# Optimization experiments

Hardware: AMD Instinct MI355X
Metric: run time of the kernel (lower is better)

## Reference

```python
import jax, jax.numpy as jnp
import numpy as np

D_IN, D, H, NE, NPATCH, B = 768, 512, 4, 2048, 49, 512
DH = D // H


def _match(q, k, w, b):
    # q:[N,Lq,D], k:[N,Lk,D] -> cross-attention of q over k, then linear proj
    s = jnp.einsum('nqd,nkd->nqk', q, k) * (q.shape[-1] ** -0.5)
    a = jax.nn.softmax(s, axis=-1)
    return jnp.einsum('nqk,nkd->nqd', a, k) @ w + b


def _mh_pool(x, query, wq, bq, wk, bk, wv, bv, wo, bo):
    # multi-head attention pooling with 1 learned query -> [N, D]
    N, P, _ = x.shape
    q = (query @ wq + bq).reshape(H, 1, DH)                      # [H,1,dh]
    k = (x @ wk + bk).reshape(N, P, H, DH).transpose(0, 2, 1, 3)  # [N,H,P,dh]
    v = (x @ wv + bv).reshape(N, P, H, DH).transpose(0, 2, 1, 3)
    s = jnp.einsum('hqd,nhkd->nhqk', q, k) * (DH ** -0.5)
    a = jax.nn.softmax(s, axis=-1)
    o = jnp.einsum('nhqk,nhkd->nhqd', a, v).transpose(0, 2, 1, 3).reshape(N, D)
    return o @ wo + bo


def _ln(x, g, b):
    m = jnp.mean(x, -1, keepdims=True)
    v = jnp.var(x, -1, keepdims=True)
    return (x - m) * jax.lax.rsqrt(v + 1e-5) * g + b


def _moe(t, i, gw, gb, tw1, tb1, tw2, tb2, iw1, ib1, iw2, ib2):
    # 2-expert softmax-gated combiner over (text, pooled image) features
    gate = jax.nn.softmax(jnp.concatenate([t, i], -1) @ gw + gb, axis=-1)  # [N,2]
    et = jax.nn.relu(t @ tw1 + tb1) @ tw2 + tb2
    ei = jax.nn.relu(i @ iw1 + ib1) @ iw2 + ib2
    return gate[:, :1] * et + gate[:, 1:] * ei


def setup_inputs():
    key = jax.random.key(0)
    ks = jax.random.split(key, 24)
    g = lambda i, sh, s=0.02: jax.random.normal(ks[i], sh, dtype=jnp.float32) * s
    z = lambda *sh: jnp.zeros(sh, jnp.float32)
    return dict(
        entity_text_cls=g(0, (NE, D_IN), 1.0),
        entity_image_tokens=g(1, (NE, NPATCH, D_IN), 1.0),
        mention_text_cls=g(2, (B, D_IN), 1.0),
        mention_image_tokens=g(3, (B, NPATCH, D_IN), 1.0),
        text_fc_w=g(4, (D_IN, D)), text_fc_b=z(D),
        image_fc_w=g(5, (D_IN, D)), image_fc_b=z(D),
        gate_fc_w=g(6, (D, 1)), gate_fc_b=z(1),
        ln_g=jnp.ones((D,), jnp.float32), ln_b=z(D),
        match_w=g(7, (D, D)), match_b=z(D),
        mh_query=g(8, (1, D)),
        mh_wq=g(9, (D, D)), mh_bq=z(D),
        mh_wk=g(10, (D, D)), mh_bk=z(D),
        mh_wv=g(11, (D, D)), mh_bv=z(D),
        mh_wo=g(12, (D, D)), mh_bo=z(D),
        moe_gw=g(13, (2 * D, 2)), moe_gb=z(2),
        moe_tw1=g(14, (D, D)), moe_tb1=z(D),
        moe_tw2=g(15, (D, D)), moe_tb2=z(D),
        moe_iw1=g(16, (D, D)), moe_ib1=z(D),
        moe_iw2=g(17, (D, D)), moe_ib2=z(D),
    )


def reference(entity_text_cls, entity_image_tokens, mention_text_cls, mention_image_tokens,
              text_fc_w, text_fc_b, image_fc_w, image_fc_b, gate_fc_w, gate_fc_b,
              ln_g, ln_b, match_w, match_b, mh_query,
              mh_wq, mh_bq, mh_wk, mh_bk, mh_wv, mh_bv, mh_wo, mh_bo,
              moe_gw, moe_gb, moe_tw1, moe_tb1, moe_tw2, moe_tb2,
              moe_iw1, moe_ib1, moe_iw2, moe_ib2):
    def side(cls, toks):
        cls_p = cls @ text_fc_w + text_fc_b          # [N,D]
        tok_p = toks @ image_fc_w + image_fc_b       # [N,P,D]
        txt = _match(cls_p[:, None, :], tok_p, match_w, match_b)[:, 0]
        img = _match(tok_p, cls_p[:, None, :], match_w, match_b)
        img = _mh_pool(img, mh_query, mh_wq, mh_bq, mh_wk, mh_bk, mh_wv, mh_bv, mh_wo, mh_bo)
        ctx = _moe(txt, img, moe_gw, moe_gb, moe_tw1, moe_tb1, moe_tw2, moe_tb2,
                   moe_iw1, moe_ib1, moe_iw2, moe_ib2)
        gate = jnp.tanh(cls_p @ gate_fc_w + gate_fc_b)
        return _ln(cls_p * gate + ctx, ln_g, ln_b)

    e_ctx = side(entity_text_cls, entity_image_tokens)   # [NE,D]
    m_ctx = side(mention_text_cls, mention_image_tokens)  # [B,D]
    return m_ctx @ e_ctx.T                                # [B,NE]
```

## Files before the change

kernel.cpp:

```cpp
#include <hip/hip_runtime.h>
#include <hip/hip_bf16.h>
#include <math.h>

namespace {
constexpr int kNE   = 2048;
constexpr int kB    = 512;
constexpr int kDin  = 768;
constexpr int kD    = 512;
constexpr int kP    = 49;
constexpr int kNtot = kNE + kB;
}

typedef __attribute__((ext_vector_type(8))) short bf16x8;
typedef __attribute__((ext_vector_type(4))) float f32x4;

__device__ inline ushort f2bf(float f) {
  unsigned u = __float_as_uint(f);
  return (ushort)((u + 0x7fffu + ((u >> 16) & 1u)) >> 16);
}
__device__ inline void split1(float v, ushort& h, ushort& l) {
  unsigned u = __float_as_uint(v);
  h = (ushort)(u >> 16);
  l = f2bf(v - __uint_as_float(u & 0xFFFF0000u));
}

struct GemmJob {
  const ushort *Ah, *Al;
  const ushort *Bh, *Bl;
  const float* bias;
  float* Cf;
  ushort *Ch, *Cl;
  int M, N, K, relu;
};
struct GemmBatch { GemmJob j[4]; int prefix[5]; };

__global__ __launch_bounds__(256) void gemm_batch(GemmBatch batch) {
  int ji = 0;
  { const int bid = blockIdx.x;
    while (ji < 3 && bid >= batch.prefix[ji + 1]) ++ji; }
  const GemmJob jb = batch.j[ji];
  const int local = blockIdx.x - batch.prefix[ji];
  const int nbx = jb.N >> 7;
  const int by = local / nbx;
  const int bx = local - by * nbx;
  const int row0 = by * 64, col0 = bx * 128;
  const int K = jb.K;
  const int nt = K >> 5;

  __shared__ ushort Ahs[2][64][40], Als[2][64][40];
  __shared__ ushort Bhs[2][128][40], Bls[2][128][40];

  const int tid  = threadIdx.x;
  const int lane = tid & 63;
  const int w    = tid >> 6;
  const int fr   = lane & 15;
  const int fk   = (lane >> 4) * 8;
  const int sr   = tid >> 2;
  const int sk   = (tid & 3) * 8;

  const ushort* pAh  = jb.Ah + (size_t)(row0 + sr) * K + sk;
  const ushort* pAl  = jb.Al + (size_t)(row0 + sr) * K + sk;
  const ushort* pBh0 = jb.Bh + (size_t)(col0 + sr) * K + sk;
  const ushort* pBl0 = jb.Bl + (size_t)(col0 + sr) * K + sk;
  const ushort* pBh1 = jb.Bh + (size_t)(col0 + 64 + sr) * K + sk;
  const ushort* pBl1 = jb.Bl + (size_t)(col0 + 64 + sr) * K + sk;

  bf16x8 rAh, rAl, rBh0, rBl0, rBh1, rBl1;
  auto LOAD = [&](int t) {
    const int o = t * 32;
    rAh  = *(const bf16x8*)(pAh + o);  rAl  = *(const bf16x8*)(pAl + o);
    rBh0 = *(const bf16x8*)(pBh0 + o); rBl0 = *(const bf16x8*)(pBl0 + o);
    rBh1 = *(const bf16x8*)(pBh1 + o); rBl1 = *(const bf16x8*)(pBl1 + o);
  };
  auto STORE = [&](int b) {
    *(bf16x8*)&Ahs[b][sr][sk] = rAh;       *(bf16x8*)&Als[b][sr][sk] = rAl;
    *(bf16x8*)&Bhs[b][sr][sk] = rBh0;      *(bf16x8*)&Bls[b][sr][sk] = rBl0;
    *(bf16x8*)&Bhs[b][64 + sr][sk] = rBh1; *(bf16x8*)&Bls[b][64 + sr][sk] = rBl1;
  };

  f32x4 acc[4][2] = {};

  LOAD(0); STORE(0);
  if (nt > 1) LOAD(1);
  __syncthreads();

  for (int t = 0; t < nt; ++t) {
    const int cur = t & 1;
    bf16x8 bh[2], bl[2];
#pragma unroll
    for (int n = 0; n < 2; ++n) {
      bh[n] = *(const bf16x8*)&Bhs[cur][w * 32 + n * 16 + fr][fk];
      bl[n] = *(const bf16x8*)&Bls[cur][w * 32 + n * 16 + fr][fk];
    }
#pragma unroll
    for (int m = 0; m < 4; ++m) {
      bf16x8 ah = *(const bf16x8*)&Ahs[cur][m * 16 + fr][fk];
      bf16x8 al = *(const bf16x8*)&Als[cur][m * 16 + fr][fk];
#pragma unroll
      for (int n = 0; n < 2; ++n) {
        acc[m][n] = __builtin_amdgcn_mfma_f32_16x16x32_bf16(ah, bh[n], acc[m][n], 0, 0, 0);
        acc[m][n] = __builtin_amdgcn_mfma_f32_16x16x32_bf16(al, bh[n], acc[m][n], 0, 0, 0);
        acc[m][n] = __builtin_amdgcn_mfma_f32_16x16x32_bf16(ah, bl[n], acc[m][n], 0, 0, 0);
      }
    }
    if (t + 1 < nt) {
      STORE(cur ^ 1);
      if (t + 2 < nt) LOAD(t + 2);
    }
    __syncthreads();
  }

  const int fq = lane >> 4;
#pragma unroll
  for (int n = 0; n < 2; ++n) {
    const int col = col0 + w * 32 + n * 16 + fr;
    const float bv = jb.bias ? jb.bias[col] : 0.f;
#pragma unroll
    for (int m = 0; m < 4; ++m) {
      const int rbase = row0 + m * 16 + fq * 4;
#pragma unroll
      for (int jj = 0; jj < 4; ++jj) {
        float v = acc[m][n][jj] + bv;
        if (jb.relu) v = fmaxf(v, 0.f);
        const size_t idx = (size_t)(rbase + jj) * jb.N + col;
        if (jb.Cf) jb.Cf[idx] = v;
        if (jb.Ch) { ushort h, l; split1(v, h, l); jb.Ch[idx] = h; jb.Cl[idx] = l; }
      }
    }
  }
}

struct SplitJob { const float* src; ushort* hi; ushort* lo; int n4; };
struct SplitArgs { SplitJob j[5]; };
__global__ __launch_bounds__(256) void split_plain(SplitArgs a) {
  const SplitJob jb = a.j[blockIdx.y];
  const int i = blockIdx.x * 256 + threadIdx.x;
  if (i >= jb.n4) return;
  float4 v = *(const float4*)&jb.src[(size_t)i * 4];
  ushort4 h, l;
  split1(v.x, h.x, l.x); split1(v.y, h.y, l.y);
  split1(v.z, h.z, l.z); split1(v.w, h.w, l.w);
  *(ushort4*)&jb.hi[(size_t)i * 4] = h;
  *(ushort4*)&jb.lo[(size_t)i * 4] = l;
}

struct TSJob { const float* src; ushort* hi; ushort* lo; int R, C; };
struct TSArgs { TSJob j[7]; };
__global__ __launch_bounds__(256) void trans_split(TSArgs a) {
  const TSJob jb = a.j[blockIdx.z];
  const int r0 = blockIdx.y * 32, c0 = blockIdx.x * 32;
  if (r0 >= jb.R || c0 >= jb.C) return;
  __shared__ float tl[32][33];
  const int tx = threadIdx.x & 31, ty = threadIdx.x >> 5;
#pragma unroll
  for (int i = 0; i < 32; i += 8)
    tl[ty + i][tx] = jb.src[(size_t)(r0 + ty + i) * jb.C + c0 + tx];
  __syncthreads();
#pragma unroll
  for (int i = 0; i < 32; i += 8) {
    ushort h, l; split1(tl[tx][ty + i], h, l);
    const size_t idx = (size_t)(c0 + ty + i) * jb.R + r0 + tx;
    jb.hi[idx] = h; jb.lo[idx] = l;
  }
}

__global__ __launch_bounds__(256) void attn_pool(
    const float* __restrict__ ent_toks, const float* __restrict__ men_toks,
    const float* __restrict__ u, ushort* __restrict__ wh, ushort* __restrict__ wl) {
  const int n = blockIdx.x;
  const float* toks = (n < kNE) ? ent_toks + (size_t)n * kP * kDin
                                : men_toks + (size_t)(n - kNE) * kP * kDin;
  const float* un = u + (size_t)n * kDin;
  const int t = threadIdx.x;
  const int lane = t & 63, wave = t >> 6;

  const float u0 = un[t], u1 = un[t + 256], u2 = un[t + 512];

  __shared__ float rs[2][4];
  float m = -INFINITY, l = 0.f, a0 = 0.f, a1 = 0.f, a2 = 0.f;
  const float scale = 0.044194173824159216f;

  for (int p = 0; p < kP; ++p) {
    const float* tp = toks + (size_t)p * kDin;
    const float t0 = tp[t], t1 = tp[t + 256], t2 = tp[t + 512];
    float d = fmaf(t0, u0, fmaf(t1, u1, t2 * u2));
    for (int o = 32; o; o >>= 1) d += __shfl_xor(d, o);
    if (lane == 0) rs[p & 1][wave] = d;
    __syncthreads();
    const float s = (rs[p & 1][0] + rs[p & 1][1] + rs[p & 1][2] + rs[p & 1][3]) * scale;
    const float mn = fmaxf(m, s);
    const float c = __expf(m - mn);
    const float e = __expf(s - mn);
    l = l * c + e;
    a0 = fmaf(a0, c, e * t0); a1 = fmaf(a1, c, e * t1); a2 = fmaf(a2, c, e * t2);
    m = mn;
  }
  const float inv = 1.f / l;
  const size_t base = (size_t)n * kDin;
  ushort h, lo2;
  split1(a0 * inv, h, lo2); wh[base + t] = h;       wl[base + t] = lo2;
  split1(a1 * inv, h, lo2); wh[base + 256 + t] = h; wl[base + 256 + t] = lo2;
  split1(a2 * inv, h, lo2); wh[base + 512 + t] = h; wl[base + 512 + t] = lo2;
}

__global__ __launch_bounds__(256) void gemv_bias(const float* __restrict__ vec,
                                                 const float* __restrict__ W,
                                                 const float* __restrict__ badd,
                                                 float* __restrict__ out, int K, int N) {
  const int j = blockIdx.x;
  const int t = threadIdx.x;
  float acc = 0.f;
  for (int k = t; k < K; k += 256) acc = fmaf(vec[k], W[(size_t)k * N + j], acc);
  for (int o = 32; o; o >>= 1) acc += __shfl_xor(acc, o);
  __shared__ float r[4];
  if ((t & 63) == 0) r[t >> 6] = acc;
  __syncthreads();
  if (t == 0) out[j] = r[0] + r[1] + r[2] + r[3] + badd[j];
}

__global__ __launch_bounds__(256) void finalize_ln(
    const float* __restrict__ cls_p, const float* __restrict__ et,
    const float* __restrict__ ei, const float* __restrict__ txt,
    const float* __restrict__ img,
    const float* __restrict__ gw, const float* __restrict__ gb,
    const float* __restrict__ gfw, const float* __restrict__ gfb,
    const float* __restrict__ lng, const float* __restrict__ lnb,
    ushort* __restrict__ ch, ushort* __restrict__ cl) {
  const int n = blockIdx.x;
  const int t = threadIdx.x;
  const int lane = t & 63, wave = t >> 6;
  const size_t base = (size_t)n * kD;
  const float c0 = cls_p[base + t], c1 = cls_p[base + 256 + t];

  const float t0 = txt[base + t], t1 = txt[base + 256 + t];
  const float i0 = img[base + t], i1 = img[base + 256 + t];
  float d  = fmaf(c0, gfw[t], c1 * gfw[t + 256]);
  float p0 = fmaf(t0, gw[t * 2 + 0], fmaf(t1, gw[(t + 256) * 2 + 0],
             fmaf(i0, gw[(512 + t) * 2 + 0], i1 * gw[(768 + t) * 2 + 0])));
  float p1 = fmaf(t0, gw[t * 2 + 1], fmaf(t1, gw[(t + 256) * 2 + 1],
             fmaf(i0, gw[(512 + t) * 2 + 1], i1 * gw[(768 + t) * 2 + 1])));
  for (int o = 32; o; o >>= 1) {
    d += __shfl_xor(d, o); p0 += __shfl_xor(p0, o); p1 += __shfl_xor(p1, o);
  }
  __shared__ float rd[4], r0[4], r1[4];
  __shared__ float gtb, g0b, g1b;
  if (lane == 0) { rd[wave] = d; r0[wave] = p0; r1[wave] = p1; }
  __syncthreads();
  if (t == 0) {
    gtb = tanhf(rd[0] + rd[1] + rd[2] + rd[3] + gfb[0]);
    const float l0 = r0[0] + r0[1] + r0[2] + r0[3] + gb[0];
    const float l1 = r1[0] + r1[1] + r1[2] + r1[3] + gb[1];
    const float mm = fmaxf(l0, l1);
    const float e0 = __expf(l0 - mm), e1 = __expf(l1 - mm);
    const float inv = 1.f / (e0 + e1);
    g0b = e0 * inv; g1b = e1 * inv;
  }
  __syncthreads();
  const float gt = gtb, g0 = g0b, g1 = g1b;

  const float y0 = c0 * gt + g0 * et[base + t]       + g1 * ei[base + t];
  const float y1 = c1 * gt + g0 * et[base + 256 + t] + g1 * ei[base + 256 + t];

  float s = y0 + y1, ss = fmaf(y0, y0, y1 * y1);
  for (int o = 32; o; o >>= 1) { s += __shfl_xor(s, o); ss += __shfl_xor(ss, o); }
  __shared__ float rsum[4], rssq[4];
  __shared__ float mb, ivb;
  if (lane == 0) { rsum[wave] = s; rssq[wave] = ss; }
  __syncthreads();
  if (t == 0) {
    const float S  = rsum[0] + rsum[1] + rsum[2] + rsum[3];
    const float SS = rssq[0] + rssq[1] + rssq[2] + rssq[3];
    const float mm = S / (float)kD;
    const float v  = SS / (float)kD - mm * mm;
    mb = mm; ivb = rsqrtf(v + 1e-5f);
  }
  __syncthreads();
  const float mm = mb, iv = ivb;
  ushort h, l;
  split1((y0 - mm) * iv * lng[t] + lnb[t], h, l);
  ch[base + t] = h; cl[base + t] = l;
  split1((y1 - mm) * iv * lng[t + 256] + lnb[t + 256], h, l);
  ch[base + 256 + t] = h; cl[base + 256 + t] = l;
}

extern "C" void kernel_launch(void* const* d_in, const int* in_sizes, int n_in,
                              void* d_out, int out_size, void* d_ws, size_t ws_size,
                              hipStream_t stream) {
  const float* ent_cls  = (const float*)d_in[0];
  const float* ent_tok  = (const float*)d_in[1];
  const float* men_cls  = (const float*)d_in[2];
  const float* men_tok  = (const float*)d_in[3];
  const float* text_w   = (const float*)d_in[4];
  const float* text_b   = (const float*)d_in[5];
  const float* img_w    = (const float*)d_in[6];
  const float* img_b    = (const float*)d_in[7];
  const float* gate_w   = (const float*)d_in[8];
  const float* gate_b   = (const float*)d_in[9];
  const float* ln_g     = (const float*)d_in[10];
  const float* ln_b     = (const float*)d_in[11];
  const float* match_w  = (const float*)d_in[12];
  const float* match_b  = (const float*)d_in[13];
  const float* mh_wv    = (const float*)d_in[19];
  const float* mh_bv    = (const float*)d_in[20];
  const float* mh_wo    = (const float*)d_in[21];
  const float* mh_bo    = (const float*)d_in[22];
  const float* moe_gw   = (const float*)d_in[23];
  const float* moe_gb   = (const float*)d_in[24];
  const float* moe_tw1  = (const float*)d_in[25];
  const float* moe_tb1  = (const float*)d_in[26];
  const float* moe_tw2  = (const float*)d_in[27];
  const float* moe_tb2  = (const float*)d_in[28];
  const float* moe_iw1  = (const float*)d_in[29];
  const float* moe_ib1  = (const float*)d_in[30];
  const float* moe_iw2  = (const float*)d_in[31];
  const float* moe_ib2  = (const float*)d_in[32];
  (void)ws_size; (void)n_in; (void)in_sizes; (void)out_size;

  char* base = (char*)d_ws;
  size_t off = 0;
  auto allocB = [&](size_t bytes) -> char* {
    char* p = base + off; off = (off + bytes + 255) & ~(size_t)255; return p;
  };
  auto allocF = [&](size_t n) { return (float*)allocB(n * 4); };
  auto allocU = [&](size_t n) { return (ushort*)allocB(n * 2); };

  float* clsp_f = allocF((size_t)kNtot * kD);
  float* u_f    = allocF((size_t)kNtot * kDin);
  float* txt_f  = allocF((size_t)kNtot * kD);
  float* img_f  = allocF((size_t)kNtot * kD);
  float* et_f   = allocF((size_t)kNtot * kD);
  float* ei_f   = allocF((size_t)kNtot * kD);
  float* bcomb  = allocF(kD);
  float* bt1    = allocF(kD);
  float* bimg   = allocF(kD);
  auto pair = [&](size_t n, ushort*& h, ushort*& l) { h = allocU(n); l = allocU(n); };
  ushort *ent_h,*ent_l,*men_h,*men_l,*imgw_h,*imgw_l,*matw_h,*matw_l,*mhwv_h,*mhwv_l;
  pair((size_t)kNE * kDin, ent_h, ent_l);
  pair((size_t)kB * kDin, men_h, men_l);
  pair((size_t)kDin * kD, imgw_h, imgw_l);
  pair((size_t)kD * kD, matw_h, matw_l);
  pair((size_t)kD * kD, mhwv_h, mhwv_l);
  ushort *textWT_h,*textWT_l,*matchWT_h,*matchWT_l,*mhWoT_h,*mhWoT_l;
  ushort *tw1T_h,*tw1T_l,*tw2T_h,*tw2T_l,*iw1T_h,*iw1T_l,*iw2T_h,*iw2T_l;
  pair((size_t)kD * kDin, textWT_h, textWT_l);
  pair((size_t)kD * kD, matchWT_h, matchWT_l);
  pair((size_t)kD * kD, mhWoT_h, mhWoT_l);
  pair((size_t)kD * kD, tw1T_h, tw1T_l);
  pair((size_t)kD * kD, tw2T_h, tw2T_l);
  pair((size_t)kD * kD, iw1T_h, iw1T_l);
  pair((size_t)kD * kD, iw2T_h, iw2T_l);
  ushort *clsp_h,*clsp_l,*U_h,*U_l,*WcombT_h,*WcombT_l,*WimgT_h,*WimgT_l;
  pair((size_t)kNtot * kD, clsp_h, clsp_l);
  pair((size_t)kD * kD, U_h, U_l);
  pair((size_t)kD * kDin, WcombT_h, WcombT_l);
  pair((size_t)kD * kD, WimgT_h, WimgT_l);
  ushort *ws_h,*ws_l,*txt_h,*txt_l,*img_h,*img_l,*ht_h,*ht_l,*hi_h,*hi_l,*ctx_h,*ctx_l;
  pair((size_t)kNtot * kDin, ws_h, ws_l);
  pair((size_t)kNtot * kD, txt_h, txt_l);
  pair((size_t)kNtot * kD, img_h, img_l);
  pair((size_t)kNtot * kD, ht_h, ht_l);
  pair((size_t)kNtot * kD, hi_h, hi_l);
  pair((size_t)kNtot * kD, ctx_h, ctx_l);

  auto nblk = [](int M, int N) { return (M / 64) * (N / 128); };
  auto launch_batch = [&](int njobs, GemmJob j0, GemmJob j1 = {}, GemmJob j2 = {},
                          GemmJob j3 = {}) {
    GemmBatch b{};
    b.j[0] = j0; b.j[1] = j1; b.j[2] = j2; b.j[3] = j3;
    b.prefix[0] = 0;
    for (int i = 0; i < 4; ++i)
      b.prefix[i + 1] = b.prefix[i] + (i < njobs ? nblk(b.j[i].M, b.j[i].N) : 0);
    hipLaunchKernelGGL(gemm_batch, dim3(b.prefix[njobs]), 256, 0, stream, b);
  };

  SplitArgs sa;
  sa.j[0] = { ent_cls, ent_h, ent_l, kNE * kDin / 4 };
  sa.j[1] = { men_cls, men_h, men_l, kB * kDin / 4 };
  sa.j[2] = { img_w,   imgw_h, imgw_l, kDin * kD / 4 };
  sa.j[3] = { match_w, matw_h, matw_l, kD * kD / 4 };
  sa.j[4] = { mh_wv,   mhwv_h, mhwv_l, kD * kD / 4 };
  hipLaunchKernelGGL(split_plain, dim3((kNE * kDin / 4 + 255) / 256, 5), 256, 0, stream, sa);

  TSArgs ta;
  ta.j[0] = { text_w,  textWT_h,  textWT_l,  kDin, kD };
  ta.j[1] = { match_w, matchWT_h, matchWT_l, kD,   kD };
  ta.j[2] = { mh_wo,   mhWoT_h,   mhWoT_l,   kD,   kD };
  ta.j[3] = { moe_tw1, tw1T_h,    tw1T_l,    kD,   kD };
  ta.j[4] = { moe_tw2, tw2T_h,    tw2T_l,    kD,   kD };
  ta.j[5] = { moe_iw1, iw1T_h,    iw1T_l,    kD,   kD };
  ta.j[6] = { moe_iw2, iw2T_h,    iw2T_l,    kD,   kD };
  hipLaunchKernelGGL(trans_split, dim3(16, 24, 7), 256, 0, stream, ta);

  hipLaunchKernelGGL(gemv_bias, dim3(kD), 256, 0, stream,
                     img_b, match_w, match_b, bcomb, kD, kD);
  hipLaunchKernelGGL(gemv_bias, dim3(kD), 256, 0, stream,
                     match_b, mh_wv, mh_bv, bt1, kD, kD);

  launch_batch(4,
    GemmJob{ ent_h, ent_l, textWT_h, textWT_l, text_b,
             clsp_f, clsp_h, clsp_l, kNE, kD, kDin, 0 },
    GemmJob{ men_h, men_l, textWT_h, textWT_l, text_b,
             clsp_f + (size_t)kNE * kD, clsp_h + (size_t)kNE * kD,
             clsp_l + (size_t)kNE * kD, kB, kD, kDin, 0 },
    GemmJob{ matchWT_h, matchWT_l, imgw_h, imgw_l, nullptr,
             nullptr, WcombT_h, WcombT_l, kD, kDin, kD, 0 },
    GemmJob{ mhWoT_h, mhWoT_l, mhwv_h, mhwv_l, nullptr,
             nullptr, U_h, U_l, kD, kD, kD, 0 });

  hipLaunchKernelGGL(gemv_bias, dim3(kD), 256, 0, stream,
                     bt1, mh_wo, mh_bo, bimg, kD, kD);

  launch_batch(2,
    GemmJob{ clsp_h, clsp_l, imgw_h, imgw_l, nullptr,
             u_f, nullptr, nullptr, kNtot, kDin, kD, 0 },
    GemmJob{ U_h, U_l, matw_h, matw_l, nullptr,
             nullptr, WimgT_h, WimgT_l, kD, kD, kD, 0 });

  hipLaunchKernelGGL(attn_pool, dim3(kNtot), 256, 0, stream,
                     ent_tok, men_tok, u_f, ws_h, ws_l);

  launch_batch(2,
    GemmJob{ ws_h, ws_l, WcombT_h, WcombT_l, bcomb,
             txt_f, txt_h, txt_l, kNtot, kD, kDin, 0 },
    GemmJob{ clsp_h, clsp_l, WimgT_h, WimgT_l, bimg,
             img_f, img_h, img_l, kNtot, kD, kD, 0 });

  launch_batch(2,
    GemmJob{ txt_h, txt_l, tw1T_h, tw1T_l, moe_tb1,
             nullptr, ht_h, ht_l, kNtot, kD, kD, 1 },
    GemmJob{ img_h, img_l, iw1T_h, iw1T_l, moe_ib1,
             nullptr, hi_h, hi_l, kNtot, kD, kD, 1 });

  launch_batch(2,
    GemmJob{ ht_h, ht_l, tw2T_h, tw2T_l, moe_tb2,
             et_f, nullptr, nullptr, kNtot, kD, kD, 0 },
    GemmJob{ hi_h, hi_l, iw2T_h, iw2T_l, moe_ib2,
             ei_f, nullptr, nullptr, kNtot, kD, kD, 0 });

  hipLaunchKernelGGL(finalize_ln, dim3(kNtot), 256, 0, stream,
                     clsp_f, et_f, ei_f, txt_f, img_f,
                     moe_gw, moe_gb, gate_w, gate_b, ln_g, ln_b, ctx_h, ctx_l);

  launch_batch(1,
    GemmJob{ ctx_h + (size_t)kNE * kD, ctx_l + (size_t)kNE * kD,
             ctx_h, ctx_l, nullptr,
             (float*)d_out, nullptr, nullptr, kB, kNE, kD, 0 });
}
```

Before: 259.2 us.

## Split-K the activation GEMMs into two halves with a separate reduce epilogue

New measurement: 342.0 us. 1.32x slower.

```diff
diff --git a/kernel.cpp b/kernel.cpp
--- a/kernel.cpp
+++ b/kernel.cpp
@@ -30,6 +30,7 @@
   const float* bias;
   float* Cf;
   ushort *Ch, *Cl;
+  float *P0, *P1;
   int M, N, K, relu;
 };
 struct GemmBatch { GemmJob j[4]; int prefix[5]; };
@@ -39,13 +40,17 @@
   { const int bid = blockIdx.x;
     while (ji < 3 && bid >= batch.prefix[ji + 1]) ++ji; }
   const GemmJob jb = batch.j[ji];
-  const int local = blockIdx.x - batch.prefix[ji];
+  int local = blockIdx.x - batch.prefix[ji];
+  int ks = 0;
+  if (jb.P0) { ks = local & 1; local >>= 1; }
   const int nbx = jb.N >> 7;
   const int by = local / nbx;
   const int bx = local - by * nbx;
   const int row0 = by * 64, col0 = bx * 128;
   const int K = jb.K;
-  const int nt = K >> 5;
+  int k_len = K, k_lo = 0;
+  if (jb.P0) { k_len = K >> 1; k_lo = ks ? k_len : 0; }
+  const int nt = k_len >> 5;
 
   __shared__ ushort Ahs[2][64][40], Als[2][64][40];
   __shared__ ushort Bhs[2][128][40], Bls[2][128][40];
@@ -58,12 +63,12 @@
   const int sr   = tid >> 2;
   const int sk   = (tid & 3) * 8;
 
-  const ushort* pAh  = jb.Ah + (size_t)(row0 + sr) * K + sk;
-  const ushort* pAl  = jb.Al + (size_t)(row0 + sr) * K + sk;
-  const ushort* pBh0 = jb.Bh + (size_t)(col0 + sr) * K + sk;
-  const ushort* pBl0 = jb.Bl + (size_t)(col0 + sr) * K + sk;
-  const ushort* pBh1 = jb.Bh + (size_t)(col0 + 64 + sr) * K + sk;
-  const ushort* pBl1 = jb.Bl + (size_t)(col0 + 64 + sr) * K + sk;
+  const ushort* pAh  = jb.Ah + (size_t)(row0 + sr) * K + k_lo + sk;
+  const ushort* pAl  = jb.Al + (size_t)(row0 + sr) * K + k_lo + sk;
+  const ushort* pBh0 = jb.Bh + (size_t)(col0 + sr) * K + k_lo + sk;
+  const ushort* pBl0 = jb.Bl + (size_t)(col0 + sr) * K + k_lo + sk;
+  const ushort* pBh1 = jb.Bh + (size_t)(col0 + 64 + sr) * K + k_lo + sk;
+  const ushort* pBl1 = jb.Bl + (size_t)(col0 + 64 + sr) * K + k_lo + sk;
 
   bf16x8 rAh, rAl, rBh0, rBl0, rBh1, rBl1;
   auto LOAD = [&](int t) {
@@ -111,21 +116,62 @@
   }
 
   const int fq = lane >> 4;
+  float* P = ks ? jb.P1 : jb.P0;
 #pragma unroll
   for (int n = 0; n < 2; ++n) {
     const int col = col0 + w * 32 + n * 16 + fr;
-    const float bv = jb.bias ? jb.bias[col] : 0.f;
+    const float bv = (!jb.P0 && jb.bias) ? jb.bias[col] : 0.f;
 #pragma unroll
     for (int m = 0; m < 4; ++m) {
       const int rbase = row0 + m * 16 + fq * 4;
 #pragma unroll
       for (int jj = 0; jj < 4; ++jj) {
-        float v = acc[m][n][jj] + bv;
-        if (jb.relu) v = fmaxf(v, 0.f);
         const size_t idx = (size_t)(rbase + jj) * jb.N + col;
-        if (jb.Cf) jb.Cf[idx] = v;
-        if (jb.Ch) { ushort h, l; split1(v, h, l); jb.Ch[idx] = h; jb.Cl[idx] = l; }
+        if (jb.P0) {
+          P[idx] = acc[m][n][jj];
+        } else {
+          float v = acc[m][n][jj] + bv;
+          if (jb.relu) v = fmaxf(v, 0.f);
+          if (jb.Cf) jb.Cf[idx] = v;
+          if (jb.Ch) { ushort h, l; split1(v, h, l); jb.Ch[idx] = h; jb.Cl[idx] = l; }
+        }
       }
+    }
+  }
+}
+
+struct RedJob { const float *s0, *s1, *bias; float* Cf; ushort *Ch, *Cl; int n4, relu; };
+struct RedBatch { RedJob j[2]; int prefix[3]; };
+
+__global__ __launch_bounds__(256) void reduce_batch(RedBatch b) {
+  const int ji = (blockIdx.x >= b.prefix[1]) ? 1 : 0;
+  const RedJob jb = b.j[ji];
+  const int local = blockIdx.x - (ji ? b.prefix[1] : 0);
+  const int base4 = local * 1024 + threadIdx.x;
+#pragma unroll
+  for (int r = 0; r < 4; ++r) {
+    const int i4 = base4 + r * 256;
+    if (i4 >= jb.n4) break;
+    const size_t e = (size_t)i4 * 4;
+    float4 a  = *(const float4*)&jb.s0[e];
+    float4 bb = *(const float4*)&jb.s1[e];
+    float4 v = make_float4(a.x + bb.x, a.y + bb.y, a.z + bb.z, a.w + bb.w);
+    if (jb.bias) {
+      const int c = (int)(e & 511);
+      v.x += jb.bias[c]; v.y += jb.bias[c + 1];
+      v.z += jb.bias[c + 2]; v.w += jb.bias[c + 3];
+    }
+    if (jb.relu) {
+      v.x = fmaxf(v.x, 0.f); v.y = fmaxf(v.y, 0.f);
+      v.z = fmaxf(v.z, 0.f); v.w = fmaxf(v.w, 0.f);
+    }
+    if (jb.Cf) *(float4*)&jb.Cf[e] = v;
+    if (jb.Ch) {
+      ushort4 h, l;
+      split1(v.x, h.x, l.x); split1(v.y, h.y, l.y);
+      split1(v.z, h.z, l.z); split1(v.w, h.w, l.w);
+      *(ushort4*)&jb.Ch[e] = h;
+      *(ushort4*)&jb.Cl[e] = l;
     }
   }
 }
@@ -161,6 +207,35 @@
     ushort h, l; split1(tl[tx][ty + i], h, l);
     const size_t idx = (size_t)(c0 + ty + i) * jb.R + r0 + tx;
     jb.hi[idx] = h; jb.lo[idx] = l;
+  }
+}
+
+__global__ __launch_bounds__(256) void bias_chain(
+    const float* __restrict__ img_b, const float* __restrict__ match_w,
+    const float* __restrict__ match_b, const float* __restrict__ mh_wv,
+    const float* __restrict__ mh_bv, const float* __restrict__ mh_wo,
+    const float* __restrict__ mh_bo, float* __restrict__ bcomb,
+    float* __restrict__ bimg) {
+  const int t = threadIdx.x;
+  if (blockIdx.x == 0) {
+    for (int j = t; j < kD; j += 256) {
+      float a = 0.f;
+      for (int k = 0; k < kD; ++k) a = fmaf(img_b[k], match_w[(size_t)k * kD + j], a);
+      bcomb[j] = a + match_b[j];
+    }
+  } else {
+    __shared__ float bt1[kD];
+    for (int j = t; j < kD; j += 256) {
+      float a = 0.f;
+      for (int k = 0; k < kD; ++k) a = fmaf(match_b[k], mh_wv[(size_t)k * kD + j], a);
+      bt1[j] = a + mh_bv[j];
+    }
+    __syncthreads();
+    for (int j = t; j < kD; j += 256) {
+      float a = 0.f;
+      for (int k = 0; k < kD; ++k) a = fmaf(bt1[k], mh_wo[(size_t)k * kD + j], a);
+      bimg[j] = a + mh_bo[j];
+    }
   }
 }
 
@@ -201,21 +276,6 @@
   split1(a0 * inv, h, lo2); wh[base + t] = h;       wl[base + t] = lo2;
   split1(a1 * inv, h, lo2); wh[base + 256 + t] = h; wl[base + 256 + t] = lo2;
   split1(a2 * inv, h, lo2); wh[base + 512 + t] = h; wl[base + 512 + t] = lo2;
-}
-
-__global__ __launch_bounds__(256) void gemv_bias(const float* __restrict__ vec,
-                                                 const float* __restrict__ W,
-                                                 const float* __restrict__ badd,
-                                                 float* __restrict__ out, int K, int N) {
-  const int j = blockIdx.x;
-  const int t = threadIdx.x;
-  float acc = 0.f;
-  for (int k = t; k < K; k += 256) acc = fmaf(vec[k], W[(size_t)k * N + j], acc);
-  for (int o = 32; o; o >>= 1) acc += __shfl_xor(acc, o);
-  __shared__ float r[4];
-  if ((t & 63) == 0) r[t >> 6] = acc;
-  __syncthreads();
-  if (t == 0) out[j] = r[0] + r[1] + r[2] + r[3] + badd[j];
 }
 
 __global__ __launch_bounds__(256) void finalize_ln(
@@ -331,8 +391,11 @@
   float* et_f   = allocF((size_t)kNtot * kD);
   float* ei_f   = allocF((size_t)kNtot * kD);
   float* bcomb  = allocF(kD);
-  float* bt1    = allocF(kD);
   float* bimg   = allocF(kD);
+  float* pp0 = allocF((size_t)kNtot * kDin);
+  float* pp1 = allocF((size_t)kNtot * kDin);
+  float* pp2 = allocF((size_t)kNtot * kDin);
+  float* pp3 = allocF((size_t)kNtot * kDin);
   auto pair = [&](size_t n, ushort*& h, ushort*& l) { h = allocU(n); l = allocU(n); };
   ushort *ent_h,*ent_l,*men_h,*men_l,*imgw_h,*imgw_l,*matw_h,*matw_l,*mhwv_h,*mhwv_l;
   pair((size_t)kNE * kDin, ent_h, ent_l);
@@ -362,15 +425,25 @@
   pair((size_t)kNtot * kD, hi_h, hi_l);
   pair((size_t)kNtot * kD, ctx_h, ctx_l);
 
-  auto nblk = [](int M, int N) { return (M / 64) * (N / 128); };
+  auto nblk = [](const GemmJob& j) {
+    return (j.M / 64) * (j.N / 128) * (j.P0 ? 2 : 1);
+  };
   auto launch_batch = [&](int njobs, GemmJob j0, GemmJob j1 = {}, GemmJob j2 = {},
                           GemmJob j3 = {}) {
     GemmBatch b{};
     b.j[0] = j0; b.j[1] = j1; b.j[2] = j2; b.j[3] = j3;
     b.prefix[0] = 0;
     for (int i = 0; i < 4; ++i)
-      b.prefix[i + 1] = b.prefix[i] + (i < njobs ? nblk(b.j[i].M, b.j[i].N) : 0);
+      b.prefix[i + 1] = b.prefix[i] + (i < njobs ? nblk(b.j[i]) : 0);
     hipLaunchKernelGGL(gemm_batch, dim3(b.prefix[njobs]), 256, 0, stream, b);
+  };
+  auto launch_reduce = [&](int njobs, RedJob j0, RedJob j1 = {}) {
+    RedBatch b{};
+    b.j[0] = j0; b.j[1] = j1;
+    b.prefix[0] = 0;
+    for (int i = 0; i < 2; ++i)
+      b.prefix[i + 1] = b.prefix[i] + (i < njobs ? (b.j[i].n4 + 1023) / 1024 : 0);
+    hipLaunchKernelGGL(reduce_batch, dim3(b.prefix[njobs]), 256, 0, stream, b);
   };
 
   SplitArgs sa;
@@ -391,51 +464,59 @@
   ta.j[6] = { moe_iw2, iw2T_h,    iw2T_l,    kD,   kD };
   hipLaunchKernelGGL(trans_split, dim3(16, 24, 7), 256, 0, stream, ta);
 
-  hipLaunchKernelGGL(gemv_bias, dim3(kD), 256, 0, stream,
-                     img_b, match_w, match_b, bcomb, kD, kD);
-  hipLaunchKernelGGL(gemv_bias, dim3(kD), 256, 0, stream,
-                     match_b, mh_wv, mh_bv, bt1, kD, kD);
+  hipLaunchKernelGGL(bias_chain, dim3(2), 256, 0, stream,
+                     img_b, match_w, match_b, mh_wv, mh_bv, mh_wo, mh_bo,
+                     bcomb, bimg);
 
   launch_batch(4,
-    GemmJob{ ent_h, ent_l, textWT_h, textWT_l, text_b,
-             clsp_f, clsp_h, clsp_l, kNE, kD, kDin, 0 },
-    GemmJob{ men_h, men_l, textWT_h, textWT_l, text_b,
-             clsp_f + (size_t)kNE * kD, clsp_h + (size_t)kNE * kD,
-             clsp_l + (size_t)kNE * kD, kB, kD, kDin, 0 },
+    GemmJob{ ent_h, ent_l, textWT_h, textWT_l, nullptr, nullptr, nullptr, nullptr,
+             pp0, pp1, kNE, kD, kDin, 0 },
+    GemmJob{ men_h, men_l, textWT_h, textWT_l, nullptr, nullptr, nullptr, nullptr,
+             pp0 + (size_t)kNE * kD, pp1 + (size_t)kNE * kD, kB, kD, kDin, 0 },
     GemmJob{ matchWT_h, matchWT_l, imgw_h, imgw_l, nullptr,
-             nullptr, WcombT_h, WcombT_l, kD, kDin, kD, 0 },
+             nullptr, WcombT_h, WcombT_l, nullptr, nullptr, kD, kDin, kD, 0 },
     GemmJob{ mhWoT_h, mhWoT_l, mhwv_h, mhwv_l, nullptr,
-             nullptr, U_h, U_l, kD, kD, kD, 0 });
-
-  hipLaunchKernelGGL(gemv_bias, dim3(kD), 256, 0, stream,
-                     bt1, mh_wo, mh_bo, bimg, kD, kD);
+             nullptr, U_h, U_l, nullptr, nullptr, kD, kD, kD, 0 });
+  launch_reduce(1, RedJob{ pp0, pp1, text_b, clsp_f, clsp_h, clsp_l,
+                           kNtot * kD / 4, 0 });
 
   launch_batch(2,
-    GemmJob{ clsp_h, clsp_l, imgw_h, imgw_l, nullptr,
-             u_f, nullptr, nullptr, kNtot, kDin, kD, 0 },
+    GemmJob{ clsp_h, clsp_l, imgw_h, imgw_l, nullptr, nullptr, nullptr, nullptr,
+             pp0, pp1, kNtot, kDin, kD, 0 },
     GemmJob{ U_h, U_l, matw_h, matw_l, nullptr,
-             nullptr, WimgT_h, WimgT_l, kD, kD, kD, 0 });
+             nullptr, WimgT_h, WimgT_l, nullptr, nullptr, kD, kD, kD, 0 });
+  launch_reduce(1, RedJob{ pp0, pp1, nullptr, u_f, nullptr, nullptr,
+                           kNtot * kDin / 4, 0 });
 
   hipLaunchKernelGGL(attn_pool, dim3(kNtot), 256, 0, stream,
                      ent_tok, men_tok, u_f, ws_h, ws_l);
 
   launch_batch(2,
-    GemmJob{ ws_h, ws_l, WcombT_h, WcombT_l, bcomb,
-             txt_f, txt_h, txt_l, kNtot, kD, kDin, 0 },
-    GemmJob{ clsp_h, clsp_l, WimgT_h, WimgT_l, bimg,
-             img_f, img_h, img_l, kNtot, kD, kD, 0 });
+    GemmJob{ ws_h, ws_l, WcombT_h, WcombT_l, nullptr, nullptr, nullptr, nullptr,
+             pp0, pp1, kNtot, kD, kDin, 0 },
+    GemmJob{ clsp_h, clsp_l, WimgT_h, WimgT_l, nullptr, nullptr, nullptr, nullptr,
+             pp2, pp3, kNtot, kD, kD, 0 });
+  launch_reduce(2,
+    RedJob{ pp0, pp1, bcomb, txt_f, txt_h, txt_l, kNtot * kD / 4, 0 },
+    RedJob{ pp2, pp3, bimg,  img_f, img_h, img_l, kNtot * kD / 4, 0 });
 
   launch_batch(2,
-    GemmJob{ txt_h, txt_l, tw1T_h, tw1T_l, moe_tb1,
-             nullptr, ht_h, ht_l, kNtot, kD, kD, 1 },
-    GemmJob{ img_h, img_l, iw1T_h, iw1T_l, moe_ib1,
-             nullptr, hi_h, hi_l, kNtot, kD, kD, 1 });
+    GemmJob{ txt_h, txt_l, tw1T_h, tw1T_l, nullptr, nullptr, nullptr, nullptr,
+             pp0, pp1, kNtot, kD, kD, 0 },
+    GemmJob{ img_h, img_l, iw1T_h, iw1T_l, nullptr, nullptr, nullptr, nullptr,
+             pp2, pp3, kNtot, kD, kD, 0 });
+  launch_reduce(2,
+    RedJob{ pp0, pp1, moe_tb1, nullptr, ht_h, ht_l, kNtot * kD / 4, 1 },
+    RedJob{ pp2, pp3, moe_ib1, nullptr, hi_h, hi_l, kNtot * kD / 4, 1 });
 
   launch_batch(2,
-    GemmJob{ ht_h, ht_l, tw2T_h, tw2T_l, moe_tb2,
-             et_f, nullptr, nullptr, kNtot, kD, kD, 0 },
-    GemmJob{ hi_h, hi_l, iw2T_h, iw2T_l, moe_ib2,
-             ei_f, nullptr, nullptr, kNtot, kD, kD, 0 });
+    GemmJob{ ht_h, ht_l, tw2T_h, tw2T_l, nullptr, nullptr, nullptr, nullptr,
+             pp0, pp1, kNtot, kD, kD, 0 },
+    GemmJob{ hi_h, hi_l, iw2T_h, iw2T_l, nullptr, nullptr, nullptr, nullptr,
+             pp2, pp3, kNtot, kD, kD, 0 });
+  launch_reduce(2,
+    RedJob{ pp0, pp1, moe_tb2, et_f, nullptr, nullptr, kNtot * kD / 4, 0 },
+    RedJob{ pp2, pp3, moe_ib2, ei_f, nullptr, nullptr, kNtot * kD / 4, 0 });
 
   hipLaunchKernelGGL(finalize_ln, dim3(kNtot), 256, 0, stream,
                      clsp_f, et_f, ei_f, txt_f, img_f,
@@ -443,6 +524,8 @@
 
   launch_batch(1,
     GemmJob{ ctx_h + (size_t)kNE * kD, ctx_l + (size_t)kNE * kD,
-             ctx_h, ctx_l, nullptr,
-             (float*)d_out, nullptr, nullptr, kB, kNE, kD, 0 });
-}
+             ctx_h, ctx_l, nullptr, nullptr, nullptr, nullptr,
+             pp0, pp1, kB, kNE, kD, 0 });
+  launch_reduce(1, RedJob{ pp0, pp1, nullptr, (float*)d_out, nullptr, nullptr,
+                           kB * kNE / 4, 0 });
+}
```

## Fuse prep kernels and precompose text and image weights to cut dependent GEMM stage

Applied to the files above, without the earlier changes.

Measured after the change: 304.6 us. +17.5%, slower.

```diff
diff --git a/kernel.cpp b/kernel.cpp
--- a/kernel.cpp
+++ b/kernel.cpp
@@ -32,12 +32,12 @@
   ushort *Ch, *Cl;
   int M, N, K, relu;
 };
-struct GemmBatch { GemmJob j[4]; int prefix[5]; };
+struct GemmBatch { GemmJob j[6]; int prefix[7]; };
 
 __global__ __launch_bounds__(256) void gemm_batch(GemmBatch batch) {
   int ji = 0;
   { const int bid = blockIdx.x;
-    while (ji < 3 && bid >= batch.prefix[ji + 1]) ++ji; }
+    while (ji < 5 && bid >= batch.prefix[ji + 1]) ++ji; }
   const GemmJob jb = batch.j[ji];
   const int local = blockIdx.x - batch.prefix[ji];
   const int nbx = jb.N >> 7;
@@ -131,36 +131,79 @@
 }
 
 struct SplitJob { const float* src; ushort* hi; ushort* lo; int n4; };
-struct SplitArgs { SplitJob j[5]; };
-__global__ __launch_bounds__(256) void split_plain(SplitArgs a) {
-  const SplitJob jb = a.j[blockIdx.y];
-  const int i = blockIdx.x * 256 + threadIdx.x;
-  if (i >= jb.n4) return;
-  float4 v = *(const float4*)&jb.src[(size_t)i * 4];
-  ushort4 h, l;
-  split1(v.x, h.x, l.x); split1(v.y, h.y, l.y);
-  split1(v.z, h.z, l.z); split1(v.w, h.w, l.w);
-  *(ushort4*)&jb.hi[(size_t)i * 4] = h;
-  *(ushort4*)&jb.lo[(size_t)i * 4] = l;
-}
-
 struct TSJob { const float* src; ushort* hi; ushort* lo; int R, C; };
-struct TSArgs { TSJob j[7]; };
-__global__ __launch_bounds__(256) void trans_split(TSArgs a) {
-  const TSJob jb = a.j[blockIdx.z];
-  const int r0 = blockIdx.y * 32, c0 = blockIdx.x * 32;
-  if (r0 >= jb.R || c0 >= jb.C) return;
+struct PrepArgs {
+  SplitJob s[6];
+  TSJob t[7];
+  const float *img_b, *match_w, *match_b, *mh_wv, *mh_bv, *mh_wo, *mh_bo;
+  const float *text_b, *img_w;
+  float *bcomb, *bimg, *b_u;
+  int prefix[17];
+};
+
+__global__ __launch_bounds__(256) void prep_all(PrepArgs a) {
+  int ji = 0;
+  { const int bid = blockIdx.x;
+    while (ji < 15 && bid >= a.prefix[ji + 1]) ++ji; }
+  const int local = blockIdx.x - a.prefix[ji];
+  const int t = threadIdx.x;
   __shared__ float tl[32][33];
-  const int tx = threadIdx.x & 31, ty = threadIdx.x >> 5;
-#pragma unroll
-  for (int i = 0; i < 32; i += 8)
-    tl[ty + i][tx] = jb.src[(size_t)(r0 + ty + i) * jb.C + c0 + tx];
-  __syncthreads();
-#pragma unroll
-  for (int i = 0; i < 32; i += 8) {
-    ushort h, l; split1(tl[tx][ty + i], h, l);
-    const size_t idx = (size_t)(c0 + ty + i) * jb.R + r0 + tx;
-    jb.hi[idx] = h; jb.lo[idx] = l;
+  __shared__ float bt1[kD];
+
+  if (ji < 6) {
+    const SplitJob jb = a.s[ji];
+    const int i = local * 256 + t;
+    if (i < jb.n4) {
+      float4 v = *(const float4*)&jb.src[(size_t)i * 4];
+      ushort4 h, l;
+      split1(v.x, h.x, l.x); split1(v.y, h.y, l.y);
+      split1(v.z, h.z, l.z); split1(v.w, h.w, l.w);
+      *(ushort4*)&jb.hi[(size_t)i * 4] = h;
+      *(ushort4*)&jb.lo[(size_t)i * 4] = l;
+    }
+  } else if (ji < 13) {
+    const TSJob jb = a.t[ji - 6];
+    const int ntx = jb.C / 32;
+    const int r0 = (local / ntx) * 32, c0 = (local % ntx) * 32;
+    const int tx = t & 31, ty = t >> 5;
+#pragma unroll
+    for (int i = 0; i < 32; i += 8)
+      tl[ty + i][tx] = jb.src[(size_t)(r0 + ty + i) * jb.C + c0 + tx];
+    __syncthreads();
+#pragma unroll
+    for (int i = 0; i < 32; i += 8) {
+      ushort h, l; split1(tl[tx][ty + i], h, l);
+      const size_t idx = (size_t)(c0 + ty + i) * jb.R + r0 + tx;
+      jb.hi[idx] = h; jb.lo[idx] = l;
+    }
+  } else if (ji == 13) {
+    for (int j = t; j < kD; j += 256) {
+      float acc = 0.f;
+      for (int k = 0; k < kD; ++k)
+        acc = fmaf(a.img_b[k], a.match_w[(size_t)k * kD + j], acc);
+      a.bcomb[j] = acc + a.match_b[j];
+    }
+  } else if (ji == 14) {
+    for (int j = t; j < kD; j += 256) {
+      float acc = 0.f;
+      for (int k = 0; k < kD; ++k)
+        acc = fmaf(a.match_b[k], a.mh_wv[(size_t)k * kD + j], acc);
+      bt1[j] = acc + a.mh_bv[j];
+    }
+    __syncthreads();
+    for (int j = t; j < kD; j += 256) {
+      float acc = 0.f;
+      for (int k = 0; k < kD; ++k)
+        acc = fmaf(bt1[k], a.mh_wo[(size_t)k * kD + j], acc);
+      a.bimg[j] = acc + a.mh_bo[j];
+    }
+  } else {
+    for (int j = t; j < kDin; j += 256) {
+      float acc = 0.f;
+      for (int k = 0; k < kD; ++k)
+        acc = fmaf(a.text_b[k], a.img_w[(size_t)j * kD + k], acc);
+      a.b_u[j] = acc;
+    }
   }
 }
 
@@ -201,21 +244,6 @@
   split1(a0 * inv, h, lo2); wh[base + t] = h;       wl[base + t] = lo2;
   split1(a1 * inv, h, lo2); wh[base + 256 + t] = h; wl[base + 256 + t] = lo2;
   split1(a2 * inv, h, lo2); wh[base + 512 + t] = h; wl[base + 512 + t] = lo2;
-}
-
-__global__ __launch_bounds__(256) void gemv_bias(const float* __restrict__ vec,
-                                                 const float* __restrict__ W,
-                                                 const float* __restrict__ badd,
-                                                 float* __restrict__ out, int K, int N) {
-  const int j = blockIdx.x;
-  const int t = threadIdx.x;
-  float acc = 0.f;
-  for (int k = t; k < K; k += 256) acc = fmaf(vec[k], W[(size_t)k * N + j], acc);
-  for (int o = 32; o; o >>= 1) acc += __shfl_xor(acc, o);
-  __shared__ float r[4];
-  if ((t & 63) == 0) r[t >> 6] = acc;
-  __syncthreads();
-  if (t == 0) out[j] = r[0] + r[1] + r[2] + r[3] + badd[j];
 }
 
 __global__ __launch_bounds__(256) void finalize_ln(
@@ -331,15 +359,17 @@
   float* et_f   = allocF((size_t)kNtot * kD);
   float* ei_f   = allocF((size_t)kNtot * kD);
   float* bcomb  = allocF(kD);
-  float* bt1    = allocF(kD);
   float* bimg   = allocF(kD);
+  float* b_u    = allocF(kDin);
   auto pair = [&](size_t n, ushort*& h, ushort*& l) { h = allocU(n); l = allocU(n); };
   ushort *ent_h,*ent_l,*men_h,*men_l,*imgw_h,*imgw_l,*matw_h,*matw_l,*mhwv_h,*mhwv_l;
+  ushort *textw_h,*textw_l;
   pair((size_t)kNE * kDin, ent_h, ent_l);
   pair((size_t)kB * kDin, men_h, men_l);
   pair((size_t)kDin * kD, imgw_h, imgw_l);
   pair((size_t)kD * kD, matw_h, matw_l);
   pair((size_t)kD * kD, mhwv_h, mhwv_l);
+  pair((size_t)kDin * kD, textw_h, textw_l);
   ushort *textWT_h,*textWT_l,*matchWT_h,*matchWT_l,*mhWoT_h,*mhWoT_l;
   ushort *tw1T_h,*tw1T_l,*tw2T_h,*tw2T_l,*iw1T_h,*iw1T_l,*iw2T_h,*iw2T_l;
   pair((size_t)kD * kDin, textWT_h, textWT_l);
@@ -350,10 +380,12 @@
   pair((size_t)kD * kD, iw1T_h, iw1T_l);
   pair((size_t)kD * kD, iw2T_h, iw2T_l);
   ushort *clsp_h,*clsp_l,*U_h,*U_l,*WcombT_h,*WcombT_l,*WimgT_h,*WimgT_l;
+  ushort *WuT_h,*WuT_l;
   pair((size_t)kNtot * kD, clsp_h, clsp_l);
   pair((size_t)kD * kD, U_h, U_l);
   pair((size_t)kD * kDin, WcombT_h, WcombT_l);
   pair((size_t)kD * kD, WimgT_h, WimgT_l);
+  pair((size_t)kDin * kDin, WuT_h, WuT_l);
   ushort *ws_h,*ws_l,*txt_h,*txt_l,*img_h,*img_l,*ht_h,*ht_l,*hi_h,*hi_l,*ctx_h,*ctx_l;
   pair((size_t)kNtot * kDin, ws_h, ws_l);
   pair((size_t)kNtot * kD, txt_h, txt_l);
@@ -362,57 +394,62 @@
   pair((size_t)kNtot * kD, hi_h, hi_l);
   pair((size_t)kNtot * kD, ctx_h, ctx_l);
 
-  auto nblk = [](int M, int N) { return (M / 64) * (N / 128); };
+  auto nblk = [](const GemmJob& j) { return (j.M / 64) * (j.N / 128); };
   auto launch_batch = [&](int njobs, GemmJob j0, GemmJob j1 = {}, GemmJob j2 = {},
-                          GemmJob j3 = {}) {
+                          GemmJob j3 = {}, GemmJob j4 = {}, GemmJob j5 = {}) {
     GemmBatch b{};
-    b.j[0] = j0; b.j[1] = j1; b.j[2] = j2; b.j[3] = j3;
+    b.j[0] = j0; b.j[1] = j1; b.j[2] = j2; b.j[3] = j3; b.j[4] = j4; b.j[5] = j5;
     b.prefix[0] = 0;
-    for (int i = 0; i < 4; ++i)
-      b.prefix[i + 1] = b.prefix[i] + (i < njobs ? nblk(b.j[i].M, b.j[i].N) : 0);
+    for (int i = 0; i < 6; ++i)
+      b.prefix[i + 1] = b.prefix[i] + (i < njobs ? nblk(b.j[i]) : 0);
     hipLaunchKernelGGL(gemm_batch, dim3(b.prefix[njobs]), 256, 0, stream, b);
   };
 
-  SplitArgs sa;
-  sa.j[0] = { ent_cls, ent_h, ent_l, kNE * kDin / 4 };
-  sa.j[1] = { men_cls, men_h, men_l, kB * kDin / 4 };
-  sa.j[2] = { img_w,   imgw_h, imgw_l, kDin * kD / 4 };
-  sa.j[3] = { match_w, matw_h, matw_l, kD * kD / 4 };
-  sa.j[4] = { mh_wv,   mhwv_h, mhwv_l, kD * kD / 4 };
-  hipLaunchKernelGGL(split_plain, dim3((kNE * kDin / 4 + 255) / 256, 5), 256, 0, stream, sa);
-
-  TSArgs ta;
-  ta.j[0] = { text_w,  textWT_h,  textWT_l,  kDin, kD };
-  ta.j[1] = { match_w, matchWT_h, matchWT_l, kD,   kD };
-  ta.j[2] = { mh_wo,   mhWoT_h,   mhWoT_l,   kD,   kD };
-  ta.j[3] = { moe_tw1, tw1T_h,    tw1T_l,    kD,   kD };
-  ta.j[4] = { moe_tw2, tw2T_h,    tw2T_l,    kD,   kD };
-  ta.j[5] = { moe_iw1, iw1T_h,    iw1T_l,    kD,   kD };
-  ta.j[6] = { moe_iw2, iw2T_h,    iw2T_l,    kD,   kD };
-  hipLaunchKernelGGL(trans_split, dim3(16, 24, 7), 256, 0, stream, ta);
-
-  hipLaunchKernelGGL(gemv_bias, dim3(kD), 256, 0, stream,
-                     img_b, match_w, match_b, bcomb, kD, kD);
-  hipLaunchKernelGGL(gemv_bias, dim3(kD), 256, 0, stream,
-                     match_b, mh_wv, mh_bv, bt1, kD, kD);
-
-  launch_batch(4,
+  PrepArgs pa{};
+  pa.s[0] = { ent_cls, ent_h, ent_l, kNE * kDin / 4 };
+  pa.s[1] = { men_cls, men_h, men_l, kB * kDin / 4 };
+  pa.s[2] = { img_w,   imgw_h, imgw_l, kDin * kD / 4 };
+  pa.s[3] = { match_w, matw_h, matw_l, kD * kD / 4 };
+  pa.s[4] = { mh_wv,   mhwv_h, mhwv_l, kD * kD / 4 };
+  pa.s[5] = { text_w,  textw_h, textw_l, kDin * kD / 4 };
+  pa.t[0] = { text_w,  textWT_h,  textWT_l,  kDin, kD };
+  pa.t[1] = { match_w, matchWT_h, matchWT_l, kD,   kD };
+  pa.t[2] = { mh_wo,   mhWoT_h,   mhWoT_l,   kD,   kD };
+  pa.t[3] = { moe_tw1, tw1T_h,    tw1T_l,    kD,   kD };
+  pa.t[4] = { moe_tw2, tw2T_h,    tw2T_l,    kD,   kD };
+  pa.t[5] = { moe_iw1, iw1T_h,    iw1T_l,    kD,   kD };
+  pa.t[6] = { moe_iw2, iw2T_h,    iw2T_l,    kD,   kD };
+  pa.img_b = img_b; pa.match_w = match_w; pa.match_b = match_b;
+  pa.mh_wv = mh_wv; pa.mh_bv = mh_bv; pa.mh_wo = mh_wo; pa.mh_bo = mh_bo;
+  pa.text_b = text_b; pa.img_w = img_w;
+  pa.bcomb = bcomb; pa.bimg = bimg; pa.b_u = b_u;
+  {
+    int pfx = 0; int c = 0;
+    pa.prefix[c++] = 0;
+    for (int i = 0; i < 6; ++i) { pfx += (pa.s[i].n4 + 255) / 256; pa.prefix[c++] = pfx; }
+    for (int i = 0; i < 7; ++i) { pfx += (pa.t[i].R / 32) * (pa.t[i].C / 32); pa.prefix[c++] = pfx; }
+    for (int i = 0; i < 3; ++i) { pfx += 1; pa.prefix[c++] = pfx; }
+    hipLaunchKernelGGL(prep_all, dim3(pfx), 256, 0, stream, pa);
+  }
+
+  launch_batch(3,
+    GemmJob{ imgw_h, imgw_l, textw_h, textw_l, nullptr,
+             nullptr, WuT_h, WuT_l, kDin, kDin, kD, 0 },
+    GemmJob{ matchWT_h, matchWT_l, imgw_h, imgw_l, nullptr,
+             nullptr, WcombT_h, WcombT_l, kD, kDin, kD, 0 },
+    GemmJob{ mhWoT_h, mhWoT_l, mhwv_h, mhwv_l, nullptr,
+             nullptr, U_h, U_l, kD, kD, kD, 0 });
+
+  launch_batch(5,
     GemmJob{ ent_h, ent_l, textWT_h, textWT_l, text_b,
              clsp_f, clsp_h, clsp_l, kNE, kD, kDin, 0 },
     GemmJob{ men_h, men_l, textWT_h, textWT_l, text_b,
              clsp_f + (size_t)kNE * kD, clsp_h + (size_t)kNE * kD,
              clsp_l + (size_t)kNE * kD, kB, kD, kDin, 0 },
-    GemmJob{ matchWT_h, matchWT_l, imgw_h, imgw_l, nullptr,
-             nullptr, WcombT_h, WcombT_l, kD, kDin, kD, 0 },
-    GemmJob{ mhWoT_h, mhWoT_l, mhwv_h, mhwv_l, nullptr,
-             nullptr, U_h, U_l, kD, kD, kD, 0 });
-
-  hipLaunchKernelGGL(gemv_bias, dim3(kD), 256, 0, stream,
-                     bt1, mh_wo, mh_bo, bimg, kD, kD);
-
-  launch_batch(2,
-    GemmJob{ clsp_h, clsp_l, imgw_h, imgw_l, nullptr,
-             u_f, nullptr, nullptr, kNtot, kDin, kD, 0 },
+    GemmJob{ ent_h, ent_l, WuT_h, WuT_l, b_u,
+             u_f, nullptr, nullptr, kNE, kDin, kDin, 0 },
+    GemmJob{ men_h, men_l, WuT_h, WuT_l, b_u,
+             u_f + (size_t)kNE * kDin, nullptr, nullptr, kB, kDin, kDin, 0 },
     GemmJob{ U_h, U_l, matw_h, matw_l, nullptr,
              nullptr, WimgT_h, WimgT_l, kD, kD, kD, 0 });
 
```
